# Kernel tuning notes

Measured on AMD Instinct MI355X. Metric: run time of the kernel, lower is better.

## Reference

```python
import jax, jax.numpy as jnp
import numpy as np

B, S, E = 4, 2048, 512
H, D = 8, 64  # n_head, attn_dim


def setup_inputs() -> dict:
    key = jax.random.key(0)
    ks = jax.random.split(key, 12)
    scale = 0.02
    return {
        "input_q": jax.random.normal(ks[0], (B, S, E), dtype=jnp.float32),
        "input_k": jax.random.normal(ks[1], (B, S, E), dtype=jnp.float32),
        "input_v": jax.random.normal(ks[2], (B, S, E), dtype=jnp.float32),
        "mask": jax.random.randint(ks[3], (B, S, S), 0, 2, dtype=jnp.int32),
        "wq": jax.random.normal(ks[4], (E, H * D), dtype=jnp.float32) * scale,
        "bq": jnp.zeros((H * D,), dtype=jnp.float32),
        "wk": jax.random.normal(ks[5], (E, H * D), dtype=jnp.float32) * scale,
        "bk": jnp.zeros((H * D,), dtype=jnp.float32),
        "wv": jax.random.normal(ks[6], (E, H * D), dtype=jnp.float32) * scale,
        "bv": jnp.zeros((H * D,), dtype=jnp.float32),
        "wo": jax.random.normal(ks[7], (H * D, E), dtype=jnp.float32) * scale,
        "bo": jnp.zeros((E,), dtype=jnp.float32),
    }


def reference(input_q, input_k, input_v, mask, wq, bq, wk, bk, wv, bv, wo, bo):
    b, lq, _ = input_q.shape
    lk = input_k.shape[1]
    # projections -> [b, len, H, D] -> [b, H, len, D]
    q = (input_q @ wq + bq).reshape(b, lq, H, D).transpose(0, 2, 1, 3)
    k = (input_k @ wk + bk).reshape(b, lk, H, D).transpose(0, 2, 1, 3)
    v = (input_v @ wv + bv).reshape(b, lk, H, D).transpose(0, 2, 1, 3)
    # raw scores [b, H, lq, lk]
    score = jnp.einsum("bhqd,bhkd->bhqk", q, k)
    # NOTE: original masks with -1e9 BEFORE dividing by sqrt(attn_dim)
    score = jnp.where(mask[:, None, :, :] == 0, jnp.float32(-1e9), score)
    attn = jax.nn.softmax(score / jnp.sqrt(jnp.float32(D)), axis=-1)
    out = jnp.einsum("bhqk,bhkd->bqhd", attn, v).reshape(b, lq, H * D)
    return out @ wo + bo
```

## Files before the change

### kernel.cpp

```cpp
#include <hip/hip_runtime.h>
#include <hip/hip_bf16.h>
#include <hip/hip_fp16.h>
#include <stdint.h>

#define Bc 4
#define Sc 2048
#define Ec 512
#define Hc 8
#define Dc 64
#define HDc 512

typedef __attribute__((ext_vector_type(8))) short bf16x8;
typedef __attribute__((ext_vector_type(4))) _Float16 f16x4;
typedef __attribute__((ext_vector_type(8))) _Float16 f16x8;
typedef __attribute__((ext_vector_type(4))) float f32x4;
typedef unsigned int u32;

__device__ __forceinline__ unsigned short f2bf(float x) {
    union { float f; unsigned u; } v; v.f = x;
    unsigned r = v.u + 0x7FFFu + ((v.u >> 16) & 1u);
    return (unsigned short)(r >> 16);
}

__device__ __forceinline__ unsigned pkbf2(float a, float b) {
    float2 f; f.x = a; f.y = b;
    __hip_bfloat162 h = __float22bfloat162_rn(f);
    union { __hip_bfloat162 h2; unsigned u; } u; u.h2 = h;
    return u.u;
}

__device__ __forceinline__ unsigned short f2h(float x) {
    return __half_as_ushort(__float2half_rn(x));
}

__device__ __forceinline__ unsigned pkh2(float a, float b) {
    union { __half2 h2; unsigned u; } u;
    u.h2 = __floats2half2_rn(a, b);
    return u.u;
}

__device__ __forceinline__ uint4 pack8(float4 a, float4 b) {
    uint4 v;
    v.x = pkbf2(a.x, a.y); v.y = pkbf2(a.z, a.w);
    v.z = pkbf2(b.x, b.y); v.w = pkbf2(b.z, b.w);
    return v;
}

__device__ __forceinline__ void gload_lds(const void* g, void* l) {
    __builtin_amdgcn_global_load_lds(
        (const __attribute__((address_space(1))) u32*)g,
        (__attribute__((address_space(3))) u32*)l,
        16, 0, 0);
}

__device__ __forceinline__ int vperm(int mt, int c) {
    return ((c >> 2) << 4) + ((mt >> 1) << 3) + ((mt & 1) << 2) + (c & 3);
}

__global__ __launch_bounds__(256) void prep(
    const int* __restrict__ mask, unsigned long long* __restrict__ bits,
    const float* __restrict__ W0, const float* __restrict__ W1,
    const float* __restrict__ W2, const float* __restrict__ W3,
    unsigned short* __restrict__ Wt,
    const float* __restrict__ Xq, const float* __restrict__ Xk,
    const float* __restrict__ Xv, unsigned short* __restrict__ Xb)
{
    const int blk = blockIdx.x;
    __shared__ float t[64][65];
    if (blk < 256) {
        const int z = blk >> 6;
        const float* W = z == 0 ? W0 : (z == 1 ? W1 : (z == 2 ? W2 : W3));
        unsigned short* O = Wt + (size_t)z * Ec * HDc;
        const int k0 = ((blk >> 3) & 7) * 64, n0 = (blk & 7) * 64;
#pragma unroll
        for (int i = 0; i < 16; i++) {
            int idx = threadIdx.x + 256 * i;
            int kr = idx >> 6, nc = idx & 63;
            t[nc][kr] = W[(size_t)(k0 + kr) * HDc + n0 + nc];
        }
        __syncthreads();
#pragma unroll
        for (int i = 0; i < 16; i++) {
            int idx = threadIdx.x + 256 * i;
            int nr = idx >> 6, kc = idx & 63;
            O[(size_t)(n0 + nr) * Ec + k0 + kc] = f2bf(t[nr][kc]);
        }
    } else if (blk < 2304) {
        const int lane = threadIdx.x & 63;
        int wave = ((blk - 256) * 256 + (int)threadIdx.x) >> 6;
        const int nwaves = (2048 * 256) >> 6;
        const int nwords = (Bc * Sc * Sc) / 64;
        for (int w = wave; w < nwords; w += nwaves) {
            int m = mask[(size_t)w * 64 + lane];
            unsigned long long b = __ballot(m != 0);
            if (lane == 0) bits[w] = b;
        }
    } else {
        const int zi = blk - 2304;
        const int z = zi >> 11, wi = zi & 2047;
        const float* X = z == 0 ? Xq : (z == 1 ? Xk : Xv);
        const size_t off = ((size_t)wi * 256 + threadIdx.x) * 8;
        const float4* p = (const float4*)(X + off);
        float4 f0 = p[0], f1 = p[1];
        *(uint4*)(Xb + (size_t)z * 4194304 + off) = pack8(f0, f1);
    }
}

__global__ __launch_bounds__(256) void proj_gemm(
    const unsigned short* __restrict__ Xb, const unsigned short* __restrict__ Wt,
    const float* __restrict__ bq, const float* __restrict__ bk, const float* __restrict__ bv,
    unsigned short* __restrict__ Oq, unsigned short* __restrict__ Ok,
    unsigned short* __restrict__ Vt)
{
    const int z = blockIdx.z;
    const unsigned short* Xz = Xb + (size_t)z * 4194304;
    const unsigned short* Bt = Wt + (size_t)z * Ec * HDc;
    const float* bias = z == 0 ? bq : (z == 1 ? bk : bv);

    const int n0 = blockIdx.x * 128;
    const int m0 = blockIdx.y * 128;
    const int tid = threadIdx.x, lane = tid & 63, w = tid >> 6;
    const int c = lane & 15, quad = lane >> 4;
    const int wm = w & 1, wn = w >> 1;

    __shared__ unsigned short As[128 * 64];
    __shared__ unsigned short Bs[128 * 64];

    f32x4 acc[4][4];
#pragma unroll
    for (int i = 0; i < 4; i++)
#pragma unroll
        for (int j = 0; j < 4; j++) acc[i][j] = (f32x4){0.f, 0.f, 0.f, 0.f};

    for (int k0 = 0; k0 < Ec; k0 += 64) {
        __syncthreads();
#pragma unroll
        for (int jj = 0; jj < 4; jj++) {
            int rb = w * 32 + jj * 8;
            int row = rb + (lane >> 3);
            int dg = (lane & 7) ^ (row & 7);
            gload_lds(Bt + (size_t)(n0 + row) * Ec + k0 + dg * 8, &Bs[rb * 64]);
            gload_lds(Xz + (size_t)(m0 + row) * Ec + k0 + dg * 8, &As[rb * 64]);
        }
        __syncthreads();
#pragma unroll
        for (int ks = 0; ks < 2; ks++) {
            int kg = ks * 4 + quad;
            bf16x8 af[4], bfr[4];
#pragma unroll
            for (int mt = 0; mt < 4; mt++) {
                int row = wm * 64 + mt * 16 + c;
                af[mt] = *(const bf16x8*)&As[row * 64 + ((kg ^ (row & 7)) * 8)];
            }
#pragma unroll
            for (int nt = 0; nt < 4; nt++) {
                int row = wn * 64 + nt * 16 + c;
                bfr[nt] = *(const bf16x8*)&Bs[row * 64 + ((kg ^ (row & 7)) * 8)];
            }
            if (z < 2) {
#pragma unroll
                for (int mt = 0; mt < 4; mt++)
#pragma unroll
                    for (int nt = 0; nt < 4; nt++)
                        acc[mt][nt] = __builtin_amdgcn_mfma_f32_16x16x32_bf16(af[mt], bfr[nt], acc[mt][nt], 0, 0, 0);
            } else {
#pragma unroll
                for (int mt = 0; mt < 4; mt++)
#pragma unroll
                    for (int nt = 0; nt < 4; nt++)
                        acc[mt][nt] = __builtin_amdgcn_mfma_f32_16x16x32_bf16(bfr[nt], af[mt], acc[mt][nt], 0, 0, 0);
            }
        }
    }

    if (z < 2) {
        unsigned short* O = z == 0 ? Oq : Ok;
        const float qs = z == 0 ? 0.125f : 1.0f;
#pragma unroll
        for (int mt = 0; mt < 4; mt++)
#pragma unroll
            for (int r = 0; r < 4; r++) {
                int gm = m0 + wm * 64 + mt * 16 + quad * 4 + r;
#pragma unroll
                for (int nt = 0; nt < 4; nt++) {
                    int gn = n0 + wn * 64 + nt * 16 + c;
                    O[(size_t)gm * HDc + gn] = f2bf((acc[mt][nt][r] + bias[gn]) * qs);
                }
            }
    } else {
#pragma unroll
        for (int mt = 0; mt < 4; mt++) {
            int gm = m0 + wm * 64 + mt * 16 + c;
            int bb = gm >> 11, sPos = gm & (Sc - 1);
            int tbase = (sPos & ~63) + vperm(mt, c);
#pragma unroll
            for (int nt = 0; nt < 4; nt++)
#pragma unroll
                for (int r = 0; r < 4; r++) {
                    int ng = n0 + wn * 64 + nt * 16 + quad * 4 + r;
                    int hh = ng >> 6, d = ng & 63;
                    Vt[((size_t)(bb * Hc + hh) * Dc + d) * Sc + tbase] = f2h(acc[mt][nt][r] + bias[ng]);
                }
        }
    }
}

__global__ __launch_bounds__(256, 4) void attn_kernel(
    const unsigned short* __restrict__ Qb, const unsigned short* __restrict__ Kb,
    const unsigned short* __restrict__ Vt, const unsigned long long* __restrict__ Mb,
    unsigned short* __restrict__ Ob)
{
    const int qt = blockIdx.x;
    const int h  = blockIdx.y;
    const int b  = blockIdx.z;
    const int q0 = qt * 64;
    const int tid = threadIdx.x, lane = tid & 63, w = tid >> 6;
    const int c = lane & 15, quad = lane >> 4;

    __shared__ unsigned short Ks[2][64 * 64];
    __shared__ unsigned short Vs[2][64 * 64];

    const int qg = q0 + w * 16 + c;
    const size_t qoff = ((size_t)b * Sc + qg) * HDc + h * Dc;

    bf16x8 qf[2];
    qf[0] = *(const bf16x8*)(Qb + qoff + quad * 8);
    qf[1] = *(const bf16x8*)(Qb + qoff + 32 + quad * 8);

    const unsigned long long* mr = Mb + ((size_t)b * Sc + qg) * (Sc / 64);
    const size_t kbase = ((size_t)b * Sc) * HDc + h * Dc;
    const size_t vbase = ((size_t)(b * Hc + h)) * Dc * Sc;

    f32x4 o[4], osum;
#pragma unroll
    for (int i = 0; i < 4; i++) o[i] = (f32x4){0.f, 0.f, 0.f, 0.f};
    osum = (f32x4){0.f, 0.f, 0.f, 0.f};

    const f16x4 ones = {(_Float16)1.0f, (_Float16)1.0f, (_Float16)1.0f, (_Float16)1.0f};

    auto stage = [&](int kt, int buf) {
#pragma unroll
        for (int j = 0; j < 2; j++) {
            int rb = w * 16 + j * 8;
            int row = rb + (lane >> 3);
            int dg = (lane & 7) ^ (row & 7);
            gload_lds(Kb + kbase + (size_t)(kt * 64 + row) * HDc + dg * 8, &Ks[buf][rb * 64]);
            gload_lds(Vt + vbase + (size_t)row * Sc + kt * 64 + dg * 8, &Vs[buf][rb * 64]);
        }
    };

    stage(0, 0);
    for (int kt = 0; kt < Sc / 64; kt++) {
        const int cur = kt & 1;
        unsigned long long mw = mr[kt];
        __syncthreads();
        if (kt + 1 < Sc / 64) stage(kt + 1, cur ^ 1);

        f32x4 s[4];
#pragma unroll
        for (int nt = 0; nt < 4; nt++) s[nt] = (f32x4){0.f, 0.f, 0.f, 0.f};
#pragma unroll
        for (int ks = 0; ks < 2; ks++) {
            int kg = ks * 4 + quad;
#pragma unroll
            for (int nt = 0; nt < 4; nt++) {
                int t = nt * 16 + c;
                bf16x8 a = *(const bf16x8*)&Ks[cur][t * 64 + ((kg ^ (t & 7)) * 8)];
                s[nt] = __builtin_amdgcn_mfma_f32_16x16x32_bf16(a, qf[ks], s[nt], 0, 0, 0);
            }
        }

        u32 mlo = (u32)(mw) >> (quad * 4);
        u32 mhi = (u32)(mw >> 32) >> (quad * 4);
        f16x4 pb[4];
#pragma unroll
        for (int nt = 0; nt < 4; nt++) {
            u32 msrc = (nt < 2) ? mlo : mhi;
            float p[4];
#pragma unroll
            for (int r = 0; r < 4; r++) {
                const int sh = (nt & 1) * 16 + r;
                int keep = ((int)(msrc << (31 - sh))) >> 31;
                float e = __expf(s[nt][r]);
                p[r] = __int_as_float(__float_as_int(e) & keep);
            }
            union { unsigned u[2]; f16x4 v; } pk;
            pk.u[0] = pkh2(p[0], p[1]);
            pk.u[1] = pkh2(p[2], p[3]);
            pb[nt] = pk.v;
        }

#pragma unroll
        for (int a = 0; a < 2; a++) {
#pragma unroll
            for (int dt = 0; dt < 4; dt++) {
                int d = dt * 16 + c;
                union { f16x8 v8; f16x4 v4[2]; } vv;
                vv.v8 = *(const f16x8*)&Vs[cur][d * 64 + (((quad * 2 + a) ^ (d & 7)) * 8)];
                o[dt] = __builtin_amdgcn_mfma_f32_16x16x16f16(vv.v4[0], pb[2*a],   o[dt], 0, 0, 0);
                o[dt] = __builtin_amdgcn_mfma_f32_16x16x16f16(vv.v4[1], pb[2*a+1], o[dt], 0, 0, 0);
            }
            osum = __builtin_amdgcn_mfma_f32_16x16x16f16(ones, pb[2*a],   osum, 0, 0, 0);
            osum = __builtin_amdgcn_mfma_f32_16x16x16f16(ones, pb[2*a+1], osum, 0, 0, 0);
        }
    }

    const float inv = 1.0f / osum[0];

#pragma unroll
    for (int dt = 0; dt < 4; dt++) {
        uint2 pk;
        pk.x = pkbf2(o[dt][0] * inv, o[dt][1] * inv);
        pk.y = pkbf2(o[dt][2] * inv, o[dt][3] * inv);
        *(uint2*)(Ob + qoff + dt * 16 + quad * 4) = pk;
    }
}

__global__ __launch_bounds__(256) void out_gemm(
    const unsigned short* __restrict__ Ab, const unsigned short* __restrict__ Bt,
    const float* __restrict__ bias, float* __restrict__ Out)
{
    const int n0 = blockIdx.x * 128;
    const int m0 = blockIdx.y * 64;
    const int tid = threadIdx.x, lane = tid & 63, w = tid >> 6;
    const int c = lane & 15, quad = lane >> 4;
    const int wm = w & 1, wn = w >> 1;

    __shared__ unsigned short As[64 * 64];
    __shared__ unsigned short Bs[128 * 64];

    f32x4 acc[2][4];
#pragma unroll
    for (int i = 0; i < 2; i++)
#pragma unroll
        for (int j = 0; j < 4; j++) acc[i][j] = (f32x4){0.f, 0.f, 0.f, 0.f};

    for (int k0 = 0; k0 < HDc; k0 += 64) {
        __syncthreads();
#pragma unroll
        for (int jj = 0; jj < 4; jj++) {
            int rb = w * 32 + jj * 8;
            int row = rb + (lane >> 3);
            int dg = (lane & 7) ^ (row & 7);
            gload_lds(Bt + (size_t)(n0 + row) * Ec + k0 + dg * 8, &Bs[rb * 64]);
        }
#pragma unroll
        for (int jj = 0; jj < 2; jj++) {
            int rb = w * 16 + jj * 8;
            int row = rb + (lane >> 3);
            int dg = (lane & 7) ^ (row & 7);
            gload_lds(Ab + (size_t)(m0 + row) * HDc + k0 + dg * 8, &As[rb * 64]);
        }
        __syncthreads();
#pragma unroll
        for (int ks = 0; ks < 2; ks++) {
            int kg = ks * 4 + quad;
            bf16x8 af[2], bfr[4];
#pragma unroll
            for (int mt = 0; mt < 2; mt++) {
                int row = wm * 32 + mt * 16 + c;
                af[mt] = *(const bf16x8*)&As[row * 64 + ((kg ^ (row & 7)) * 8)];
            }
#pragma unroll
            for (int nt = 0; nt < 4; nt++) {
                int row = wn * 64 + nt * 16 + c;
                bfr[nt] = *(const bf16x8*)&Bs[row * 64 + ((kg ^ (row & 7)) * 8)];
            }
#pragma unroll
            for (int mt = 0; mt < 2; mt++)
#pragma unroll
                for (int nt = 0; nt < 4; nt++)
                    acc[mt][nt] = __builtin_amdgcn_mfma_f32_16x16x32_bf16(af[mt], bfr[nt], acc[mt][nt], 0, 0, 0);
        }
    }
#pragma unroll
    for (int mt = 0; mt < 2; mt++)
#pragma unroll
        for (int r = 0; r < 4; r++) {
            int gm = m0 + wm * 32 + mt * 16 + quad * 4 + r;
#pragma unroll
            for (int nt = 0; nt < 4; nt++) {
                int gn = n0 + wn * 64 + nt * 16 + c;
                Out[(size_t)gm * Ec + gn] = acc[mt][nt][r] + bias[gn];
            }
        }
}

extern "C" void kernel_launch(void* const* d_in, const int* in_sizes, int n_in,
                              void* d_out, int out_size, void* d_ws, size_t ws_size,
                              hipStream_t stream)
{
    const float* xq = (const float*)d_in[0];
    const float* xk = (const float*)d_in[1];
    const float* xv = (const float*)d_in[2];
    const int* mask = (const int*)d_in[3];
    const float* wq = (const float*)d_in[4];
    const float* bq = (const float*)d_in[5];
    const float* wk = (const float*)d_in[6];
    const float* bk = (const float*)d_in[7];
    const float* wv = (const float*)d_in[8];
    const float* bv = (const float*)d_in[9];
    const float* wo = (const float*)d_in[10];
    const float* bo = (const float*)d_in[11];
    float* out = (float*)d_out;

    char* ws = (char*)d_ws;
    const size_t MB = 1024 * 1024;
    unsigned short* qb = (unsigned short*)(ws + 0 * MB);
    unsigned short* kb = (unsigned short*)(ws + 8 * MB);
    unsigned short* vt = (unsigned short*)(ws + 16 * MB);
    unsigned short* xb = (unsigned short*)(ws + 24 * MB);
    unsigned short* ab = (unsigned short*)(ws + 24 * MB);
    unsigned long long* mb = (unsigned long long*)(ws + 48 * MB);
    unsigned short* wt = (unsigned short*)(ws + 50 * MB);

    hipLaunchKernelGGL(prep, dim3(8448), dim3(256), 0, stream,
                       mask, mb, wq, wk, wv, wo, wt, xq, xk, xv, xb);

    hipLaunchKernelGGL(proj_gemm, dim3(4, 64, 3), dim3(256), 0, stream,
                       xb, wt, bq, bk, bv, qb, kb, vt);

    hipLaunchKernelGGL(attn_kernel, dim3(32, 8, 4), dim3(256), 0, stream,
                       qb, kb, vt, mb, ab);

    hipLaunchKernelGGL(out_gemm, dim3(4, 128), dim3(256), 0, stream,
                       ab, wt + 3 * (size_t)Ec * HDc, bo, out);
}
```

Baseline: 271.3 us.

## Switch attention to 32x32 MFMA tiles with 128-query blocks

Rewrites the attention inner loop to use 32x32x16 bf16/f16 MFMAs, with each wave covering 32 queries and each block covering 128 queries. K/V tiles loaded into LDS are now reused by twice as many queries. The row sum is computed with fdot2 on the packed probabilities instead of an extra MFMA against ones, and a lane shuffle rearranges P into the B-operand layout. V is now stored unpermuted. The grid halves and launch bounds drop to 2 blocks per CU, which cuts occupancy and raises register pressure.

```diff
diff --git a/kernel.cpp b/kernel.cpp
--- a/kernel.cpp
+++ b/kernel.cpp
@@ -11,9 +11,11 @@
 #define HDc 512
 
 typedef __attribute__((ext_vector_type(8))) short bf16x8;
+typedef __attribute__((ext_vector_type(2))) _Float16 f16x2;
 typedef __attribute__((ext_vector_type(4))) _Float16 f16x4;
 typedef __attribute__((ext_vector_type(8))) _Float16 f16x8;
 typedef __attribute__((ext_vector_type(4))) float f32x4;
+typedef __attribute__((ext_vector_type(16))) float f32x16;
 typedef unsigned int u32;
 
 __device__ __forceinline__ unsigned short f2bf(float x) {
@@ -51,10 +53,6 @@
         (const __attribute__((address_space(1))) u32*)g,
         (__attribute__((address_space(3))) u32*)l,
         16, 0, 0);
-}
-
-__device__ __forceinline__ int vperm(int mt, int c) {
-    return ((c >> 2) << 4) + ((mt >> 1) << 3) + ((mt & 1) << 2) + (c & 3);
 }
 
 __global__ __launch_bounds__(256) void prep(
@@ -192,51 +190,50 @@
         for (int mt = 0; mt < 4; mt++) {
             int gm = m0 + wm * 64 + mt * 16 + c;
             int bb = gm >> 11, sPos = gm & (Sc - 1);
-            int tbase = (sPos & ~63) + vperm(mt, c);
 #pragma unroll
             for (int nt = 0; nt < 4; nt++)
 #pragma unroll
                 for (int r = 0; r < 4; r++) {
                     int ng = n0 + wn * 64 + nt * 16 + quad * 4 + r;
                     int hh = ng >> 6, d = ng & 63;
-                    Vt[((size_t)(bb * Hc + hh) * Dc + d) * Sc + tbase] = f2h(acc[mt][nt][r] + bias[ng]);
+                    Vt[((size_t)(bb * Hc + hh) * Dc + d) * Sc + sPos] = f2h(acc[mt][nt][r] + bias[ng]);
                 }
         }
     }
 }
 
-__global__ __launch_bounds__(256, 4) void attn_kernel(
+__global__ __launch_bounds__(256, 2) void attn_kernel(
     const unsigned short* __restrict__ Qb, const unsigned short* __restrict__ Kb,
     const unsigned short* __restrict__ Vt, const unsigned long long* __restrict__ Mb,
     unsigned short* __restrict__ Ob)
 {
     const int qt = blockIdx.x;
-    const int h  = blockIdx.y;
+    const int hb = blockIdx.y;
     const int b  = blockIdx.z;
-    const int q0 = qt * 64;
+    const int q0 = qt * 128;
     const int tid = threadIdx.x, lane = tid & 63, w = tid >> 6;
-    const int c = lane & 15, quad = lane >> 4;
+    const int l31 = lane & 31, hf = lane >> 5;
 
     __shared__ unsigned short Ks[2][64 * 64];
     __shared__ unsigned short Vs[2][64 * 64];
 
-    const int qg = q0 + w * 16 + c;
-    const size_t qoff = ((size_t)b * Sc + qg) * HDc + h * Dc;
-
-    bf16x8 qf[2];
-    qf[0] = *(const bf16x8*)(Qb + qoff + quad * 8);
-    qf[1] = *(const bf16x8*)(Qb + qoff + 32 + quad * 8);
+    const int qg = q0 + w * 32 + l31;
+    const size_t qoff = ((size_t)b * Sc + qg) * HDc + hb * Dc;
+
+    bf16x8 qf[4];
+#pragma unroll
+    for (int s4 = 0; s4 < 4; s4++)
+        qf[s4] = *(const bf16x8*)(Qb + qoff + s4 * 16 + hf * 8);
 
     const unsigned long long* mr = Mb + ((size_t)b * Sc + qg) * (Sc / 64);
-    const size_t kbase = ((size_t)b * Sc) * HDc + h * Dc;
-    const size_t vbase = ((size_t)(b * Hc + h)) * Dc * Sc;
-
-    f32x4 o[4], osum;
-#pragma unroll
-    for (int i = 0; i < 4; i++) o[i] = (f32x4){0.f, 0.f, 0.f, 0.f};
-    osum = (f32x4){0.f, 0.f, 0.f, 0.f};
-
-    const f16x4 ones = {(_Float16)1.0f, (_Float16)1.0f, (_Float16)1.0f, (_Float16)1.0f};
+    const size_t kbase = ((size_t)b * Sc) * HDc + hb * Dc;
+    const size_t vbase = ((size_t)(b * Hc + hb)) * Dc * Sc;
+
+    f32x16 o[2];
+#pragma unroll
+    for (int i = 0; i < 16; i++) { o[0][i] = 0.f; o[1][i] = 0.f; }
+    float os[4] = {0.f, 0.f, 0.f, 0.f};
+    const f16x2 one2 = {(_Float16)1.0f, (_Float16)1.0f};
 
     auto stage = [&](int kt, int buf) {
 #pragma unroll
@@ -256,64 +253,77 @@
         __syncthreads();
         if (kt + 1 < Sc / 64) stage(kt + 1, cur ^ 1);
 
-        f32x4 s[4];
-#pragma unroll
-        for (int nt = 0; nt < 4; nt++) s[nt] = (f32x4){0.f, 0.f, 0.f, 0.f};
-#pragma unroll
-        for (int ks = 0; ks < 2; ks++) {
-            int kg = ks * 4 + quad;
-#pragma unroll
-            for (int nt = 0; nt < 4; nt++) {
-                int t = nt * 16 + c;
-                bf16x8 a = *(const bf16x8*)&Ks[cur][t * 64 + ((kg ^ (t & 7)) * 8)];
-                s[nt] = __builtin_amdgcn_mfma_f32_16x16x32_bf16(a, qf[ks], s[nt], 0, 0, 0);
-            }
-        }
-
-        u32 mlo = (u32)(mw) >> (quad * 4);
-        u32 mhi = (u32)(mw >> 32) >> (quad * 4);
-        f16x4 pb[4];
-#pragma unroll
-        for (int nt = 0; nt < 4; nt++) {
-            u32 msrc = (nt < 2) ? mlo : mhi;
-            float p[4];
-#pragma unroll
-            for (int r = 0; r < 4; r++) {
-                const int sh = (nt & 1) * 16 + r;
-                int keep = ((int)(msrc << (31 - sh))) >> 31;
-                float e = __expf(s[nt][r]);
-                p[r] = __int_as_float(__float_as_int(e) & keep);
-            }
-            union { unsigned u[2]; f16x4 v; } pk;
-            pk.u[0] = pkh2(p[0], p[1]);
-            pk.u[1] = pkh2(p[2], p[3]);
-            pb[nt] = pk.v;
-        }
-
+        u32 P16[2][8];
 #pragma unroll
         for (int a = 0; a < 2; a++) {
-#pragma unroll
-            for (int dt = 0; dt < 4; dt++) {
-                int d = dt * 16 + c;
-                union { f16x8 v8; f16x4 v4[2]; } vv;
-                vv.v8 = *(const f16x8*)&Vs[cur][d * 64 + (((quad * 2 + a) ^ (d & 7)) * 8)];
-                o[dt] = __builtin_amdgcn_mfma_f32_16x16x16f16(vv.v4[0], pb[2*a],   o[dt], 0, 0, 0);
-                o[dt] = __builtin_amdgcn_mfma_f32_16x16x16f16(vv.v4[1], pb[2*a+1], o[dt], 0, 0, 0);
-            }
-            osum = __builtin_amdgcn_mfma_f32_16x16x16f16(ones, pb[2*a],   osum, 0, 0, 0);
-            osum = __builtin_amdgcn_mfma_f32_16x16x16f16(ones, pb[2*a+1], osum, 0, 0, 0);
+            f32x16 s;
+#pragma unroll
+            for (int i = 0; i < 16; i++) s[i] = 0.f;
+            const int t = a * 32 + l31;
+#pragma unroll
+            for (int s4 = 0; s4 < 4; s4++) {
+                bf16x8 kf = *(const bf16x8*)&Ks[cur][t * 64 + (((2 * s4 + hf) ^ (t & 7)) * 8)];
+                s = __builtin_amdgcn_mfma_f32_32x32x16_bf16(kf, qf[s4], s, 0, 0, 0);
+            }
+            u32 mwa = (a == 0) ? (u32)mw : (u32)(mw >> 32);
+            u32 mq = mwa >> (4 * hf);
+#pragma unroll
+            for (int g = 0; g < 4; g++) {
+                float p[4];
+#pragma unroll
+                for (int r = 0; r < 4; r++) {
+                    const int pos = 8 * g + r;
+                    int keep = ((int)(mq << (31 - pos))) >> 31;
+                    float e = __expf(s[4 * g + r]);
+                    p[r] = __int_as_float(__float_as_int(e) & keep);
+                }
+                u32 u0 = pkh2(p[0], p[1]);
+                u32 u1 = pkh2(p[2], p[3]);
+                P16[a][2 * g + 0] = u0;
+                P16[a][2 * g + 1] = u1;
+                union { u32 u; f16x2 h; } d0, d1;
+                d0.u = u0; d1.u = u1;
+                os[g] = __builtin_amdgcn_fdot2(d0.h, one2, os[g], false);
+                os[g] = __builtin_amdgcn_fdot2(d1.h, one2, os[g], false);
+            }
+        }
+
+#pragma unroll
+        for (int s4 = 0; s4 < 4; s4++) {
+            const int a = s4 >> 1, base = 4 * (s4 & 1);
+            union { u32 u[4]; f16x8 v; } pf;
+#pragma unroll
+            for (int pp = 0; pp < 2; pp++) {
+                u32 A0 = P16[a][base + pp];
+                u32 B1 = P16[a][base + 2 + pp];
+                u32 sent = hf ? A0 : B1;
+                u32 got = (u32)__shfl_xor((int)sent, 32, 64);
+                pf.u[pp]     = hf ? got : A0;
+                pf.u[2 + pp] = hf ? B1  : got;
+            }
+#pragma unroll
+            for (int dt = 0; dt < 2; dt++) {
+                const int d = dt * 32 + l31;
+                f16x8 vf = *(const f16x8*)&Vs[cur][d * 64 + (((2 * s4 + hf) ^ (d & 7)) * 8)];
+                o[dt] = __builtin_amdgcn_mfma_f32_32x32x16_f16(vf, pf.v, o[dt], 0, 0, 0);
+            }
         }
     }
 
-    const float inv = 1.0f / osum[0];
-
-#pragma unroll
-    for (int dt = 0; dt < 4; dt++) {
-        uint2 pk;
-        pk.x = pkbf2(o[dt][0] * inv, o[dt][1] * inv);
-        pk.y = pkbf2(o[dt][2] * inv, o[dt][3] * inv);
-        *(uint2*)(Ob + qoff + dt * 16 + quad * 4) = pk;
-    }
+    float osum = os[0] + os[1] + os[2] + os[3];
+    osum += __shfl_xor(osum, 32, 64);
+    const float inv = 1.0f / osum;
+
+#pragma unroll
+    for (int dt = 0; dt < 2; dt++)
+#pragma unroll
+        for (int g = 0; g < 4; g++) {
+            const int d = dt * 32 + 8 * g + 4 * hf;
+            uint2 pk;
+            pk.x = pkbf2(o[dt][4 * g + 0] * inv, o[dt][4 * g + 1] * inv);
+            pk.y = pkbf2(o[dt][4 * g + 2] * inv, o[dt][4 * g + 3] * inv);
+            *(uint2*)(Ob + qoff + d) = pk;
+        }
 }
 
 __global__ __launch_bounds__(256) void out_gemm(
@@ -420,7 +430,7 @@
     hipLaunchKernelGGL(proj_gemm, dim3(4, 64, 3), dim3(256), 0, stream,
                        xb, wt, bq, bk, bv, qb, kb, vt);
 
-    hipLaunchKernelGGL(attn_kernel, dim3(32, 8, 4), dim3(256), 0, stream,
+    hipLaunchKernelGGL(attn_kernel, dim3(16, 8, 4), dim3(256), 0, stream,
                        qb, kb, vt, mb, ab);
 
     hipLaunchKernelGGL(out_gemm, dim3(4, 128), dim3(256), 0, stream,
```

New measurement: 276.7 us. No clear change (+2.0%).
